# Kernel tuning notes

Measured on AMD Instinct MI355X. Metric: run time of the kernel, lower is better.

## Reference

```python
import jax, jax.numpy as jnp
import numpy as np

T, B, D, H = 256, 256, 512, 1024


def setup_inputs() -> dict:
    key = jax.random.key(0)
    ks = jax.random.split(key, 9)
    s = 0.02  # small init scale for numerical sanity
    return {
        "inputs": jax.random.normal(ks[0], (T, B, D), dtype=jnp.float32),
        "Wf": jax.random.normal(ks[1], (D + H, H), dtype=jnp.float32) * s,
        "bf": jax.random.normal(ks[2], (H,), dtype=jnp.float32) * s,
        "Wi": jax.random.normal(ks[3], (D + H, H), dtype=jnp.float32) * s,
        "bi": jax.random.normal(ks[4], (H,), dtype=jnp.float32) * s,
        "Wg": jax.random.normal(ks[5], (D + H, H), dtype=jnp.float32) * s,
        "bg": jax.random.normal(ks[6], (H,), dtype=jnp.float32) * s,
        "Wo": jax.random.normal(ks[7], (D + H, H), dtype=jnp.float32) * s,
        "bo": jax.random.normal(ks[8], (H,), dtype=jnp.float32) * s,
    }


def reference(inputs, Wf, bf, Wi, bi, Wg, bg, Wo, bo):
    hidden_dim = Wf.shape[1]
    batch = inputs.shape[1]
    # Fuse the four gate projections into one [D+H, 4H] GEMM per step.
    W = jnp.concatenate([Wf, Wi, Wg, Wo], axis=1)   # [D+H, 4H]
    b = jnp.concatenate([bf, bi, bg, bo], axis=0)   # [4H]

    h0 = jnp.zeros((batch, hidden_dim), dtype=inputs.dtype)
    c0 = jnp.zeros((batch, hidden_dim), dtype=inputs.dtype)

    def step(carry, x):
        hx, cx = carry
        combined = jnp.concatenate([x, hx], axis=1)  # [B, D+H]
        z = combined @ W + b                          # [B, 4H]
        f, i, g, o = jnp.split(z, 4, axis=1)
        f = jax.nn.sigmoid(f)
        i = jax.nn.sigmoid(i)
        g = jnp.tanh(g)
        o = jax.nn.sigmoid(o)
        cx = f * cx + i * g
        hx = o * jnp.tanh(cx)
        return (hx, cx), hx

    (hx, cx), outputs = jax.lax.scan(step, (h0, c0), inputs)
    return outputs, hx, cx
```

## Files before the change

### kernel.cpp

```cpp
#include <hip/hip_runtime.h>
#include <cstdint>
#include <cstddef>

#define T_STEPS 256
#define BATCH   256
#define DIN     512
#define HID     1024
#define KTOT    1536
#define NOUT    4096
#define BHSZ    ((size_t)BATCH * HID)

typedef __bf16 bf16;
typedef __bf16 bf16x4 __attribute__((ext_vector_type(4)));
typedef __bf16 bf16x8 __attribute__((ext_vector_type(8)));
typedef float  f32x4  __attribute__((ext_vector_type(4)));

__device__ __forceinline__ void store_bf16_sc(bf16* p, bf16 v) {
  unsigned short u = __builtin_bit_cast(unsigned short, v);
  asm volatile("global_store_short %0, %1, off sc0 sc1" :: "v"(p), "v"(u) : "memory");
}

#define VMW_(N) asm volatile("s_waitcnt vmcnt(" #N ")" ::: "memory")
#define VMW(N) do { VMW_(N); __builtin_amdgcn_sched_barrier(0); } while (0)
#define LGKM0() do { asm volatile("s_waitcnt lgkmcnt(0)" ::: "memory"); \
                     __builtin_amdgcn_sched_barrier(0); } while (0)
#define SBAR() __builtin_amdgcn_sched_barrier(0)
#define RAWBAR() do { SBAR(); __builtin_amdgcn_s_barrier(); SBAR(); } while (0)

__device__ __forceinline__ float fexp2(float x) {
  float r; asm("v_exp_f32 %0, %1" : "=v"(r) : "v"(x)); return r;
}
__device__ __forceinline__ float frcp(float x) {
  float r; asm("v_rcp_f32 %0, %1" : "=v"(r) : "v"(x)); return r;
}
__device__ __forceinline__ float fsigmoid(float x) {
  return frcp(1.f + fexp2(-1.44269504f * x));
}
__device__ __forceinline__ float ftanh(float x) {
  return 1.f - 2.f * frcp(1.f + fexp2(2.88539008f * x));
}

__global__ void convert_w_kernel(const float* __restrict__ Wf, const float* __restrict__ Wi,
                                 const float* __restrict__ Wg, const float* __restrict__ Wo,
                                 bf16* __restrict__ Wt) {
  __shared__ float tile[64][17];
  const int k0 = blockIdx.x * 64;
  const int jb = blockIdx.y;
  const int j0 = jb * 16;
  const int t  = threadIdx.x;
  const float* srcs[4] = {Wf, Wi, Wg, Wo};
#pragma unroll
  for (int g = 0; g < 4; ++g) {
    const float* src = srcs[g];
    {
      const int jl = t & 15, kb = t >> 4;
#pragma unroll
      for (int r = 0; r < 4; ++r) {
        const int kl = kb + 16 * r;
        tile[kl][jl] = src[(size_t)(k0 + kl) * HID + (j0 + jl)];
      }
    }
    __syncthreads();
    {
      const int kk = t & 63, jl4 = t >> 6;
#pragma unroll
      for (int r = 0; r < 4; ++r) {
        const int jl = jl4 + 4 * r;
        Wt[(size_t)(jb * 64 + g * 16 + jl) * KTOT + (k0 + kk)] = (bf16)tile[kk][jl];
      }
    }
    __syncthreads();
  }
}

__global__ void convert_x_kernel(const float* __restrict__ X, bf16* __restrict__ xb) {
  const int t = blockIdx.y;
  const int i = blockIdx.x * blockDim.x + threadIdx.x;
  const float4 v = ((const float4*)(X + (size_t)t * BATCH * DIN))[i];
  bf16x4 o;
  o[0] = (bf16)v.x; o[1] = (bf16)v.y; o[2] = (bf16)v.z; o[3] = (bf16)v.w;
  ((bf16x4*)(xb + (size_t)t * BATCH * DIN))[i] = o;
}

__global__ __launch_bounds__(512, 2)
void lstm_v12(const bf16* __restrict__ Bt,
              const bf16* __restrict__ xb,
              bf16* __restrict__ hseq,
              const bf16* __restrict__ zb16,
              float* __restrict__ outF,
              const float* __restrict__ bf_, const float* __restrict__ bi_,
              const float* __restrict__ bg_, const float* __restrict__ bo_,
              unsigned* __restrict__ flags) {
  __shared__ f32x4 redu[8][16][64];

  const int tid = threadIdx.x, lane = tid & 63, wid = tid >> 6;
  const int bid = blockIdx.x;
  const int e8  = bid & 7;
  const int mblk = e8 >> 1;
  const int nblk = ((bid >> 3) << 1) | (e8 & 1);
  const int bm0 = mblk * 64;
  const int bn0 = nblk * 64;
  const int fr = lane & 15, fq = lane >> 4;

  if (tid == 0)
    (void)__hip_atomic_load(flags, __ATOMIC_ACQUIRE, __HIP_MEMORY_SCOPE_AGENT);
  __syncthreads();

  const int j = nblk * 16 + fr;
  const float bfv = bf_[j], biv = bi_[j], bgv = bg_[j], bov = bo_[j];
  float cr[2] = {0.f, 0.f};

  bf16x8 breg[6][4];
#pragma unroll
  for (int s = 0; s < 6; ++s) {
    const int ks = wid + 8 * s;
#pragma unroll
    for (int nf = 0; nf < 4; ++nf)
      breg[s][nf] = *(const bf16x8*)(Bt + (size_t)(bn0 + nf * 16 + fr) * KTOT
                                     + ks * 32 + fq * 8);
  }

  bf16x8 S0[4], S1[4], S2[4], S3[4];

  auto ldx = [&](int t2, int s, bf16x8 (&slot)[4]) {
    const bf16* src = xb + (size_t)t2 * BATCH * DIN + (wid + 8 * s) * 32 + fq * 8;
#pragma unroll
    for (int mf = 0; mf < 4; ++mf)
      slot[mf] = *(const bf16x8*)(src + (size_t)(bm0 + mf * 16 + fr) * DIN);
  };
  auto ldh = [&](int t2, int s, bf16x8 (&slot)[4]) {
    const int c0 = (wid + 8 * s) * 32 - 512;
    const int pp = (c0 >> 4) + (fq >> 1);
    const bf16* base = (t2 == 0)
        ? zb16
        : hseq + (((size_t)(t2 - 1) << 8) + mblk * 64 + pp) * 1024;
    const int coloff = (fq & 1) * 8;
#pragma unroll
    for (int mf = 0; mf < 4; ++mf)
      slot[mf] = *(const bf16x8*)(base + (mf * 16 + fr) * 16 + coloff);
  };

  const int pn8 = 2 * wid + ((lane & 7) >> 1) * 16 + (lane & 1);
  auto poll = [&](int tprev) {
    const unsigned* f = flags + (size_t)tprev * 256 + mblk * 64 + pn8;
    const unsigned long long tt0 = __builtin_amdgcn_s_memrealtime();
    for (;;) {
      unsigned v = __hip_atomic_load(f, __ATOMIC_RELAXED,
                                     __HIP_MEMORY_SCOPE_AGENT);
      if (__all(v != 0)) break;
      __builtin_amdgcn_s_sleep(1);
      if (__builtin_amdgcn_s_memrealtime() - tt0 > (1ULL << 22)) break;
    }
    asm volatile("" ::: "memory");
    __builtin_amdgcn_sched_barrier(0);
  };

#define MFMA16(ACC, SLOT, S) do {                                           \
    __builtin_amdgcn_s_setprio(1);                                          \
    _Pragma("unroll")                                                       \
    for (int mf_ = 0; mf_ < 4; ++mf_) {                                     \
      _Pragma("unroll")                                                     \
      for (int nf_ = 0; nf_ < 4; ++nf_)                                     \
        ACC[mf_][nf_] = __builtin_amdgcn_mfma_f32_16x16x32_bf16(            \
            SLOT[mf_], breg[S][nf_], ACC[mf_][nf_], 0, 0, 0);               \
    }                                                                       \
    __builtin_amdgcn_s_setprio(0);                                          \
  } while (0)

#define STEP(T0, XA, XB, HA, HB, HC, HD, NA, NB) do {                       \
    const int t_ = (T0);                                                    \
    f32x4 acc[4][4] = {};                                                   \
    VMW(4);  MFMA16(acc, XA, 0);                                            \
    VMW(0);  MFMA16(acc, XB, 1);                                            \
    if (t_ > 0) poll(t_ - 1);                    \
    ldh(t_, 2, HA); ldh(t_, 3, HB); ldh(t_, 4, HC); ldh(t_, 5, HD); SBAR(); \
    VMW(12); MFMA16(acc, HA, 2);                                            \
    VMW(8);  MFMA16(acc, HB, 3);                                            \
    VMW(4);  MFMA16(acc, HC, 4);                                            \
    VMW(0);  MFMA16(acc, HD, 5);                                            \
                      \
    _Pragma("unroll")                                                       \
    for (int mf_ = 0; mf_ < 4; ++mf_) {                                     \
      _Pragma("unroll")                                                     \
      for (int nf_ = 0; nf_ < 4; ++nf_)                                     \
        redu[wid][mf_ * 4 + nf_][lane] = acc[mf_][nf_];                     \
    }                                                                       \
    LGKM0();                                                                \
    RAWBAR();                                                               \
    const int mfo_ = wid >> 1;                                              \
    float hv_[2];                                                           \
    _Pragma("unroll")                                                       \
    for (int e_ = 0; e_ < 2; ++e_) {                                        \
         \
      const int lsel_ = (((wid & 1) << 1) + e_) * 16 + fr;                  \
      float z_[4];                                                          \
      _Pragma("unroll")                                                     \
      for (int nf_ = 0; nf_ < 4; ++nf_) {                                   \
        float sum_ = 0.f;                                                   \
        _Pragma("unroll")                                                   \
        for (int s_ = 0; s_ < 8; ++s_)                                      \
          sum_ += ((const float*)&redu[s_][mfo_ * 4 + nf_][lsel_])[fq];     \
        z_[nf_] = sum_;                                                     \
      }                                                                     \
      const float fg_ = fsigmoid(z_[0] + bfv);                              \
      const float ig_ = fsigmoid(z_[1] + biv);                              \
      const float gg_ = ftanh(z_[2] + bgv);                                 \
      const float og_ = fsigmoid(z_[3] + bov);                              \
      cr[e_] = fg_ * cr[e_] + ig_ * gg_;                                    \
      hv_[e_] = og_ * ftanh(cr[e_]);                                        \
    }                                                                       \
           \
    bf16* tile_ = hseq + (((size_t)t_ << 8) + mblk * 64 + nblk) * 1024;     \
    store_bf16_sc(&tile_[wid * 128 + lane], (bf16)hv_[0]);                  \
    store_bf16_sc(&tile_[wid * 128 + 64 + lane], (bf16)hv_[1]);             \
    float* outSl_ = outF + (size_t)t_ * BHSZ;                               \
    _Pragma("unroll")                                                       \
    for (int e_ = 0; e_ < 2; ++e_) {                                        \
      const size_t off_ = (size_t)(bm0 + wid * 8 + e_ * 4 + fq) * HID + j;  \
      outSl_[off_] = hv_[e_];                                               \
      if (t_ == T_STEPS - 1)                                                \
        outF[(size_t)(T_STEPS + 1) * BHSZ + off_] = cr[e_];                 \
    }                                                                       \
    if (t_ + 1 < T_STEPS) {                                                 \
      ldx(t_ + 1, 0, NA); ldx(t_ + 1, 1, NB); SBAR();                       \
      VMW(10);         \
    } else {                                                                \
      VMW(0);                                                               \
    }                                                                       \
    RAWBAR();                                                               \
    if (tid == 0)                                                           \
      __hip_atomic_store(&flags[(size_t)t_ * 256 + mblk * 64 + nblk], 1u,   \
                         __ATOMIC_RELAXED, __HIP_MEMORY_SCOPE_AGENT);       \
  } while (0)

  ldx(0, 0, S0); SBAR();
  ldx(0, 1, S1); SBAR();

#pragma unroll 1
  for (int t = 0; t < T_STEPS; t += 2) {
    STEP(t,     S0, S1, S2, S3, S0, S1, S2, S3);
    STEP(t + 1, S2, S3, S0, S1, S2, S3, S0, S1);
  }
#undef STEP
#undef MFMA16
}

__global__ __launch_bounds__(512, 2)
void lstm_fb(const bf16* __restrict__ Bt,
             const float* __restrict__ X,
             const float* __restrict__ zbF,
             float* __restrict__ outF,
             const float* __restrict__ bf_, const float* __restrict__ bi_,
             const float* __restrict__ bg_, const float* __restrict__ bo_,
             unsigned* __restrict__ flags) {
  __shared__ f32x4 redu[8][16][64];
  const int tid = threadIdx.x, lane = tid & 63, wid = tid >> 6;
  const int bid = blockIdx.x;
  const int xcd = bid & 7, sl = bid >> 3;
  const int nblk = xcd * 8 + (sl & 7);
  const int mblk = sl >> 3;
  const int bm0 = mblk * 64;
  const int bn0 = nblk * 64;
  const int fr = lane & 15, fq = lane >> 4;

  if (tid == 0)
    (void)__hip_atomic_load(flags, __ATOMIC_ACQUIRE, __HIP_MEMORY_SCOPE_AGENT);
  __syncthreads();

  const int j = nblk * 16 + fr;
  const float bfv = bf_[j], biv = bi_[j], bgv = bg_[j], bov = bo_[j];
  float cr[2] = {0.f, 0.f};

  bf16x8 breg[6][4];
#pragma unroll
  for (int s = 0; s < 6; ++s) {
    const int ks = wid + 8 * s;
#pragma unroll
    for (int nf = 0; nf < 4; ++nf)
      breg[s][nf] = *(const bf16x8*)(Bt + (size_t)(bn0 + nf * 16 + fr) * KTOT
                                     + ks * 32 + fq * 8);
  }

  bf16x8 afp[2][4];

  auto poll = [&](int tprev) {
    const unsigned* f = flags + (size_t)tprev * 256 + mblk * 64;
    const unsigned long long tt0 = __builtin_amdgcn_s_memrealtime();
    for (;;) {
      unsigned v = __hip_atomic_load(f + lane, __ATOMIC_RELAXED,
                                     __HIP_MEMORY_SCOPE_AGENT);
      if (__all(v != 0)) break;
      __builtin_amdgcn_s_sleep(2);
      if (__builtin_amdgcn_s_memrealtime() - tt0 > (1ULL << 22)) break;
    }
    asm volatile("" ::: "memory");
    __builtin_amdgcn_sched_barrier(0);
  };

  auto loadA = [&](int t2, int s, int p) __attribute__((always_inline)) {
    const int ks = wid + 8 * s;
    const int k = ks * 32 + fq * 8;
    if (s == 2 && t2 > 0) poll(t2 - 1);
    const float* src; int ld, kk;
    if (s < 2) { src = X + (size_t)t2 * BATCH * DIN; ld = DIN; kk = k; }
    else {
      src = (t2 == 0) ? zbF : outF + (size_t)(t2 - 1) * BHSZ;
      ld = HID; kk = k - 512;
    }
#pragma unroll
    for (int mf = 0; mf < 4; ++mf) {
      const float* q = src + (size_t)(bm0 + mf * 16 + fr) * ld + kk;
      const f32x4 lo = *(const f32x4*)q;
      const f32x4 hi = *(const f32x4*)(q + 4);
      bf16x8 v;
      v[0] = (bf16)lo[0]; v[1] = (bf16)lo[1]; v[2] = (bf16)lo[2]; v[3] = (bf16)lo[3];
      v[4] = (bf16)hi[0]; v[5] = (bf16)hi[1]; v[6] = (bf16)hi[2]; v[7] = (bf16)hi[3];
      afp[p][mf] = v;
    }
  };

  loadA(0, 0, 0);

#pragma unroll 1
  for (int t = 0; t < T_STEPS; ++t) {
    f32x4 acc[4][4] = {};
#pragma unroll
    for (int s = 0; s < 6; ++s) {
      if (s < 5)                loadA(t, s + 1, (s + 1) & 1);
      else if (t + 1 < T_STEPS) loadA(t + 1, 0, 0);
      __builtin_amdgcn_s_setprio(1);
#pragma unroll
      for (int mf = 0; mf < 4; ++mf)
#pragma unroll
        for (int nf = 0; nf < 4; ++nf)
          acc[mf][nf] = __builtin_amdgcn_mfma_f32_16x16x32_bf16(
              afp[s & 1][mf], breg[s][nf], acc[mf][nf], 0, 0, 0);
      __builtin_amdgcn_s_setprio(0);
    }

#pragma unroll
    for (int mf = 0; mf < 4; ++mf)
#pragma unroll
      for (int nf = 0; nf < 4; ++nf)
        redu[wid][mf * 4 + nf][lane] = acc[mf][nf];
    __syncthreads();

    const int fbase = (wid >> 1) * 4;
    const int rh = wid & 1;
    float z[2][4];
#pragma unroll
    for (int e = 0; e < 2; ++e) {
      const int rloc = rh * 8 + fq * 2 + e;
      const int lsel = (rloc >> 2) * 16 + fr;
      const int rc = rloc & 3;
#pragma unroll
      for (int nf = 0; nf < 4; ++nf) {
        float sum = 0.f;
#pragma unroll
        for (int s = 0; s < 8; ++s)
          sum += ((const float*)&redu[s][fbase + nf][lsel])[rc];
        z[e][nf] = sum;
      }
    }

    float* outSl = outF + (size_t)t * BHSZ;
#pragma unroll
    for (int e = 0; e < 2; ++e) {
      const float fg = 1.f / (1.f + expf(-(z[e][0] + bfv)));
      const float ig = 1.f / (1.f + expf(-(z[e][1] + biv)));
      const float gg = tanhf(z[e][2] + bgv);
      const float og = 1.f / (1.f + expf(-(z[e][3] + bov)));
      cr[e] = fg * cr[e] + ig * gg;
      const float h = og * tanhf(cr[e]);
      const int m = bm0 + wid * 8 + fq * 2 + e;
      const size_t off = (size_t)m * HID + j;
      __hip_atomic_store(&outSl[off], h, __ATOMIC_RELAXED,
                         __HIP_MEMORY_SCOPE_AGENT);
      if (t == T_STEPS - 1)
        outF[(size_t)(T_STEPS + 1) * BHSZ + off] = cr[e];
    }
    asm volatile("s_waitcnt vmcnt(0)" ::: "memory");
    __syncthreads();
    if (tid == 0)
      __hip_atomic_store(&flags[(size_t)t * 256 + mblk * 64 + nblk], 1u,
                         __ATOMIC_RELAXED, __HIP_MEMORY_SCOPE_AGENT);
  }
}

extern "C" void kernel_launch(void* const* d_in, const int* in_sizes, int n_in,
                              void* d_out, int out_size, void* d_ws, size_t ws_size,
                              hipStream_t stream) {
  const float* X   = (const float*)d_in[0];
  const float* Wf  = (const float*)d_in[1];
  const float* bf_ = (const float*)d_in[2];
  const float* Wi  = (const float*)d_in[3];
  const float* bi_ = (const float*)d_in[4];
  const float* Wg  = (const float*)d_in[5];
  const float* bg_ = (const float*)d_in[6];
  const float* Wo  = (const float*)d_in[7];
  const float* bo_ = (const float*)d_in[8];
  float* out = (float*)d_out;

  const size_t WtB   = (size_t)NOUT * KTOT * 2;
  const size_t zBb   = BHSZ * 4;
  const size_t flagB = (size_t)T_STEPS * 256 * 4;
  const size_t XbB   = (size_t)T_STEPS * BATCH * DIN * 2;
  const size_t HsB   = (size_t)T_STEPS * 256 * 1024 * 2;

  char* ws = (char*)d_ws;
  bf16*     Wt    = (bf16*)ws;              ws += WtB;
  float*    zbF   = (float*)(void*)ws;      ws += zBb;
  unsigned* flags = (unsigned*)(void*)ws;   ws += flagB;

  const bool big = ws_size >= WtB + zBb + flagB + XbB + HsB + (1u << 20);
  bf16* xbp = nullptr;  bf16* hseq = nullptr;
  if (big) {
    xbp  = (bf16*)ws;   ws += XbB;
    hseq = (bf16*)ws;
  }

  hipMemsetAsync(zbF, 0, zBb + flagB, stream);

  convert_w_kernel<<<dim3(KTOT / 64, NOUT / 64), 256, 0, stream>>>(Wf, Wi, Wg, Wo, Wt);

  if (big) {
    convert_x_kernel<<<dim3(BATCH * DIN / 4 / 256, T_STEPS), 256, 0, stream>>>(X, xbp);
    lstm_v12<<<256, 512, 0, stream>>>(Wt, xbp, hseq, (const bf16*)zbF, out,
                                      bf_, bi_, bg_, bo_, flags);
  } else {
    lstm_fb<<<256, 512, 0, stream>>>(Wt, X, zbF, out,
                                     bf_, bi_, bg_, bo_, flags);
  }

  hipMemcpyAsync(out + (size_t)T_STEPS * BHSZ, out + (size_t)(T_STEPS - 1) * BHSZ,
                 BHSZ * 4, hipMemcpyDeviceToDevice, stream);
}
```

Measured before the change: 2.062 ms.

## Split batch into two halves to overlap recurrent sync with compute

Each workgroup now handles two 32-row batch halves instead of one 64-row block. It gets separate per-half flags and h tiles, so half A's gate finish, h store and flag publish can overlap with half B's recurrent MFMAs. The goal is to hide the inter-block polling and reduction latency on the per-timestep critical path. In exchange there are more flag polls and barriers per step, smaller MFMA batches, and a new hseq/flag layout.

```diff
diff --git a/kernel.cpp b/kernel.cpp
--- a/kernel.cpp
+++ b/kernel.cpp
@@ -83,7 +83,7 @@
 }
 
 __global__ __launch_bounds__(512, 2)
-void lstm_v12(const bf16* __restrict__ Bt,
+void lstm_v13(const bf16* __restrict__ Bt,
               const bf16* __restrict__ xb,
               bf16* __restrict__ hseq,
               const bf16* __restrict__ zb16,
@@ -91,16 +91,16 @@
               const float* __restrict__ bf_, const float* __restrict__ bi_,
               const float* __restrict__ bg_, const float* __restrict__ bo_,
               unsigned* __restrict__ flags) {
-  __shared__ f32x4 redu[8][16][64];
+  __shared__ f32x4 redu[8][8][64];
 
   const int tid = threadIdx.x, lane = tid & 63, wid = tid >> 6;
   const int bid = blockIdx.x;
   const int e8  = bid & 7;
-  const int mblk = e8 >> 1;
+  const int mh   = e8 >> 1;
   const int nblk = ((bid >> 3) << 1) | (e8 & 1);
-  const int bm0 = mblk * 64;
   const int bn0 = nblk * 64;
   const int fr = lane & 15, fq = lane >> 4;
+  const int rowA = mh * 32, rowB = 128 + mh * 32;
 
   if (tid == 0)
     (void)__hip_atomic_load(flags, __ATOMIC_ACQUIRE, __HIP_MEMORY_SCOPE_AGENT);
@@ -108,7 +108,7 @@
 
   const int j = nblk * 16 + fr;
   const float bfv = bf_[j], biv = bi_[j], bgv = bg_[j], bov = bo_[j];
-  float cr[2] = {0.f, 0.f};
+  float crA = 0.f, crB = 0.f;
 
   bf16x8 breg[6][4];
 #pragma unroll
@@ -120,29 +120,29 @@
                                      + ks * 32 + fq * 8);
   }
 
-  bf16x8 S0[4], S1[4], S2[4], S3[4];
-
-  auto ldx = [&](int t2, int s, bf16x8 (&slot)[4]) {
+  bf16x8 xA0[2], xA1[2], xB0[2], xB1[2], h2[2], h3[2], h4[2], h5[2];
+
+  auto ldx = [&](int t2, int rowbase, int s, bf16x8 (&sl)[2]) {
     const bf16* src = xb + (size_t)t2 * BATCH * DIN + (wid + 8 * s) * 32 + fq * 8;
 #pragma unroll
-    for (int mf = 0; mf < 4; ++mf)
-      slot[mf] = *(const bf16x8*)(src + (size_t)(bm0 + mf * 16 + fr) * DIN);
-  };
-  auto ldh = [&](int t2, int s, bf16x8 (&slot)[4]) {
+    for (int mf = 0; mf < 2; ++mf)
+      sl[mf] = *(const bf16x8*)(src + (size_t)(rowbase + mf * 16 + fr) * DIN);
+  };
+  auto ldh = [&](int t2, int half, int s, bf16x8 (&sl)[2]) {
     const int c0 = (wid + 8 * s) * 32 - 512;
     const int pp = (c0 >> 4) + (fq >> 1);
     const bf16* base = (t2 == 0)
         ? zb16
-        : hseq + (((size_t)(t2 - 1) << 8) + mblk * 64 + pp) * 1024;
+        : hseq + ((((size_t)(t2 - 1) * 2 + half) << 8) + mh * 64 + pp) * 512;
     const int coloff = (fq & 1) * 8;
 #pragma unroll
-    for (int mf = 0; mf < 4; ++mf)
-      slot[mf] = *(const bf16x8*)(base + (mf * 16 + fr) * 16 + coloff);
+    for (int mf = 0; mf < 2; ++mf)
+      sl[mf] = *(const bf16x8*)(base + (mf * 16 + fr) * 16 + coloff);
   };
 
   const int pn8 = 2 * wid + ((lane & 7) >> 1) * 16 + (lane & 1);
-  auto poll = [&](int tprev) {
-    const unsigned* f = flags + (size_t)tprev * 256 + mblk * 64 + pn8;
+  auto pollh = [&](int tprev, int half) {
+    const unsigned* f = flags + (((size_t)tprev * 2 + half) << 8) + mh * 64 + pn8;
     const unsigned long long tt0 = __builtin_amdgcn_s_memrealtime();
     for (;;) {
       unsigned v = __hip_atomic_load(f, __ATOMIC_RELAXED,
@@ -155,94 +155,101 @@
     __builtin_amdgcn_sched_barrier(0);
   };
 
-#define MFMA16(ACC, SLOT, S) do {                                           \
+  auto dump = [&](f32x4 (&acc)[2][4]) {
+#pragma unroll
+    for (int mf = 0; mf < 2; ++mf)
+#pragma unroll
+      for (int nf = 0; nf < 4; ++nf)
+        redu[wid][mf * 4 + nf][lane] = acc[mf][nf];
+  };
+
+  auto finish = [&](int t2, int half, float& cre) {
+    const int mf_c = wid >> 2;
+    const int lsel = (wid & 3) * 16 + fr;
+    float z[4];
+#pragma unroll
+    for (int nf = 0; nf < 4; ++nf) {
+      float s_ = 0.f;
+#pragma unroll
+      for (int s = 0; s < 8; ++s)
+        s_ += ((const float*)&redu[s][mf_c * 4 + nf][lsel])[fq];
+      z[nf] = s_;
+    }
+    const float fg = fsigmoid(z[0] + bfv);
+    const float ig = fsigmoid(z[1] + biv);
+    const float gg = ftanh(z[2] + bgv);
+    const float og = fsigmoid(z[3] + bov);
+    cre = fg * cre + ig * gg;
+    const float h = og * ftanh(cre);
+    bf16* tile = hseq + ((((size_t)t2 * 2 + half) << 8) + mh * 64 + nblk) * 512;
+    store_bf16_sc(&tile[wid * 64 + lane], (bf16)h);
+    const int rowg = half * 128 + mh * 32 + wid * 4 + fq;
+    outF[(size_t)t2 * BHSZ + (size_t)rowg * HID + j] = h;
+    if (t2 == T_STEPS - 1)
+      outF[(size_t)(T_STEPS + 1) * BHSZ + (size_t)rowg * HID + j] = cre;
+  };
+
+  auto setflag = [&](int t2, int half) {
+    __hip_atomic_store(&flags[(((size_t)t2 * 2 + half) << 8) + mh * 64 + nblk],
+                       1u, __ATOMIC_RELAXED, __HIP_MEMORY_SCOPE_AGENT);
+  };
+
+#define MFMA8(ACC, SL, S) do {                                              \
     __builtin_amdgcn_s_setprio(1);                                          \
     _Pragma("unroll")                                                       \
-    for (int mf_ = 0; mf_ < 4; ++mf_) {                                     \
+    for (int mf_ = 0; mf_ < 2; ++mf_) {                                     \
       _Pragma("unroll")                                                     \
       for (int nf_ = 0; nf_ < 4; ++nf_)                                     \
         ACC[mf_][nf_] = __builtin_amdgcn_mfma_f32_16x16x32_bf16(            \
-            SLOT[mf_], breg[S][nf_], ACC[mf_][nf_], 0, 0, 0);               \
+            SL[mf_], breg[S][nf_], ACC[mf_][nf_], 0, 0, 0);                 \
     }                                                                       \
     __builtin_amdgcn_s_setprio(0);                                          \
   } while (0)
 
-#define STEP(T0, XA, XB, HA, HB, HC, HD, NA, NB) do {                       \
-    const int t_ = (T0);                                                    \
-    f32x4 acc[4][4] = {};                                                   \
-    VMW(4);  MFMA16(acc, XA, 0);                                            \
-    VMW(0);  MFMA16(acc, XB, 1);                                            \
-    if (t_ > 0) poll(t_ - 1);                    \
-    ldh(t_, 2, HA); ldh(t_, 3, HB); ldh(t_, 4, HC); ldh(t_, 5, HD); SBAR(); \
-    VMW(12); MFMA16(acc, HA, 2);                                            \
-    VMW(8);  MFMA16(acc, HB, 3);                                            \
-    VMW(4);  MFMA16(acc, HC, 4);                                            \
-    VMW(0);  MFMA16(acc, HD, 5);                                            \
-                      \
-    _Pragma("unroll")                                                       \
-    for (int mf_ = 0; mf_ < 4; ++mf_) {                                     \
-      _Pragma("unroll")                                                     \
-      for (int nf_ = 0; nf_ < 4; ++nf_)                                     \
-        redu[wid][mf_ * 4 + nf_][lane] = acc[mf_][nf_];                     \
-    }                                                                       \
-    LGKM0();                                                                \
-    RAWBAR();                                                               \
-    const int mfo_ = wid >> 1;                                              \
-    float hv_[2];                                                           \
-    _Pragma("unroll")                                                       \
-    for (int e_ = 0; e_ < 2; ++e_) {                                        \
-         \
-      const int lsel_ = (((wid & 1) << 1) + e_) * 16 + fr;                  \
-      float z_[4];                                                          \
-      _Pragma("unroll")                                                     \
-      for (int nf_ = 0; nf_ < 4; ++nf_) {                                   \
-        float sum_ = 0.f;                                                   \
-        _Pragma("unroll")                                                   \
-        for (int s_ = 0; s_ < 8; ++s_)                                      \
-          sum_ += ((const float*)&redu[s_][mfo_ * 4 + nf_][lsel_])[fq];     \
-        z_[nf_] = sum_;                                                     \
-      }                                                                     \
-      const float fg_ = fsigmoid(z_[0] + bfv);                              \
-      const float ig_ = fsigmoid(z_[1] + biv);                              \
-      const float gg_ = ftanh(z_[2] + bgv);                                 \
-      const float og_ = fsigmoid(z_[3] + bov);                              \
-      cr[e_] = fg_ * cr[e_] + ig_ * gg_;                                    \
-      hv_[e_] = og_ * ftanh(cr[e_]);                                        \
-    }                                                                       \
-           \
-    bf16* tile_ = hseq + (((size_t)t_ << 8) + mblk * 64 + nblk) * 1024;     \
-    store_bf16_sc(&tile_[wid * 128 + lane], (bf16)hv_[0]);                  \
-    store_bf16_sc(&tile_[wid * 128 + 64 + lane], (bf16)hv_[1]);             \
-    float* outSl_ = outF + (size_t)t_ * BHSZ;                               \
-    _Pragma("unroll")                                                       \
-    for (int e_ = 0; e_ < 2; ++e_) {                                        \
-      const size_t off_ = (size_t)(bm0 + wid * 8 + e_ * 4 + fq) * HID + j;  \
-      outSl_[off_] = hv_[e_];                                               \
-      if (t_ == T_STEPS - 1)                                                \
-        outF[(size_t)(T_STEPS + 1) * BHSZ + off_] = cr[e_];                 \
-    }                                                                       \
-    if (t_ + 1 < T_STEPS) {                                                 \
-      ldx(t_ + 1, 0, NA); ldx(t_ + 1, 1, NB); SBAR();                       \
-      VMW(10);         \
-    } else {                                                                \
-      VMW(0);                                                               \
-    }                                                                       \
-    RAWBAR();                                                               \
-    if (tid == 0)                                                           \
-      __hip_atomic_store(&flags[(size_t)t_ * 256 + mblk * 64 + nblk], 1u,   \
-                         __ATOMIC_RELAXED, __HIP_MEMORY_SCOPE_AGENT);       \
-  } while (0)
-
-  ldx(0, 0, S0); SBAR();
-  ldx(0, 1, S1); SBAR();
+  ldx(0, rowA, 0, xA0); SBAR(); ldx(0, rowA, 1, xA1); SBAR();
+  ldx(0, rowB, 0, xB0); SBAR(); ldx(0, rowB, 1, xB1); SBAR();
+  VMW(4);
 
 #pragma unroll 1
-  for (int t = 0; t < T_STEPS; t += 2) {
-    STEP(t,     S0, S1, S2, S3, S0, S1, S2, S3);
-    STEP(t + 1, S2, S3, S0, S1, S2, S3, S0, S1);
-  }
-#undef STEP
-#undef MFMA16
+  for (int t = 0; t < T_STEPS; ++t) {
+    f32x4 accA[2][4] = {}, accB[2][4] = {};
+    MFMA8(accA, xA0, 0); MFMA8(accA, xA1, 1);
+    if (t > 0) pollh(t - 1, 0);
+    ldh(t, 0, 2, h2); SBAR(); ldh(t, 0, 3, h3); SBAR();
+    ldh(t, 0, 4, h4); SBAR(); ldh(t, 0, 5, h5); SBAR();
+    VMW(8);
+    MFMA8(accB, xB0, 0); MFMA8(accB, xB1, 1);
+    VMW(6); MFMA8(accA, h2, 2);
+    VMW(4); MFMA8(accA, h3, 3);
+    VMW(2); MFMA8(accA, h4, 4);
+    VMW(0); MFMA8(accA, h5, 5);
+    dump(accA); LGKM0(); RAWBAR();
+    if (t > 0) pollh(t - 1, 1);
+    ldh(t, 1, 2, h2); SBAR(); ldh(t, 1, 3, h3); SBAR();
+    ldh(t, 1, 4, h4); SBAR(); ldh(t, 1, 5, h5); SBAR();
+    finish(t, 0, crA);
+    if (t + 1 < T_STEPS) {
+      ldx(t + 1, rowA, 0, xA0); SBAR(); ldx(t + 1, rowA, 1, xA1); SBAR();
+      VMW(5);
+    } else {
+      VMW(0);
+    }
+    RAWBAR();
+    if (tid == 0) setflag(t, 0);
+    MFMA8(accB, h2, 2); MFMA8(accB, h3, 3);
+    MFMA8(accB, h4, 4); MFMA8(accB, h5, 5);
+    dump(accB); LGKM0(); RAWBAR();
+    finish(t, 1, crB);
+    if (t + 1 < T_STEPS) {
+      ldx(t + 1, rowB, 0, xB0); SBAR(); ldx(t + 1, rowB, 1, xB1); SBAR();
+      VMW(4);
+    } else {
+      VMW(0);
+    }
+    RAWBAR();
+    if (tid == 0) setflag(t, 1);
+  }
+#undef MFMA8
 }
 
 __global__ __launch_bounds__(512, 2)
@@ -403,9 +410,9 @@
 
   const size_t WtB   = (size_t)NOUT * KTOT * 2;
   const size_t zBb   = BHSZ * 4;
-  const size_t flagB = (size_t)T_STEPS * 256 * 4;
+  const size_t flagB = (size_t)T_STEPS * 2 * 256 * 4;
   const size_t XbB   = (size_t)T_STEPS * BATCH * DIN * 2;
-  const size_t HsB   = (size_t)T_STEPS * 256 * 1024 * 2;
+  const size_t HsB   = (size_t)T_STEPS * 2 * 256 * 1024;
 
   char* ws = (char*)d_ws;
   bf16*     Wt    = (bf16*)ws;              ws += WtB;
@@ -425,7 +432,7 @@
 
   if (big) {
     convert_x_kernel<<<dim3(BATCH * DIN / 4 / 256, T_STEPS), 256, 0, stream>>>(X, xbp);
-    lstm_v12<<<256, 512, 0, stream>>>(Wt, xbp, hseq, (const bf16*)zbF, out,
+    lstm_v13<<<256, 512, 0, stream>>>(Wt, xbp, hseq, (const bf16*)zbF, out,
                                       bf_, bi_, bg_, bo_, flags);
   } else {
     lstm_fb<<<256, 512, 0, stream>>>(Wt, X, zbF, out,
```

Measured after the change: 1.903 ms (median of 2 runs). -7.7%, faster.
